# Performance work log

Measured on AMD Instinct MI355X. Metric: run time of the kernel, lower is better.

The kernel has to match this reference:

```python
import jax, jax.numpy as jnp
import numpy as np

H = 8          # n_heads
M = 16         # max_dist
U = 512        # n_units
DH = U // H    # d_head
EPS = 1e-3     # keras LayerNormalization default epsilon
NEG = -2.0**32 + 1.0


def _rel_table(pe, T):
    # pe: [2M+1, DH]; returns [T, T, DH] with rel[i, j] = pe[clip(j - i, -M, M) + M]
    i = jnp.arange(T)
    idx = jnp.clip(i[None, :] - i[:, None], -M, M) + M
    return pe[idx]


def _split_heads(x):
    # [B, T, U] -> [H*B, T, DH]  (head-major, matching tf.concat(tf.split(x, H, 2), 0))
    B, T, _ = x.shape
    return x.reshape(B, T, H, DH).transpose(2, 0, 1, 3).reshape(H * B, T, DH)


def _merge_heads(x, B):
    # [H*B, T, DH] -> [B, T, U]
    T = x.shape[1]
    return x.reshape(H, B, T, DH).transpose(1, 2, 0, 3).reshape(B, T, U)


def setup_inputs() -> dict:
    key = jax.random.key(0)
    ks = jax.random.split(key, 10)
    B, T = 8, 1024
    s = 1.0 / np.sqrt(U)
    inp = {
        'q': jax.random.normal(ks[0], (B, T, U), jnp.float32),
        'k': jax.random.normal(ks[1], (B, T, U), jnp.float32),
        'v': jax.random.normal(ks[2], (B, T, U), jnp.float32),
        'Wq': jax.random.normal(ks[3], (U, U), jnp.float32) * s,
        'bq': jnp.zeros((U,), jnp.float32),
        'Wk': jax.random.normal(ks[4], (U, U), jnp.float32) * s,
        'bk': jnp.zeros((U,), jnp.float32),
        'Wv': jax.random.normal(ks[5], (U, U), jnp.float32) * s,
        'bv': jnp.zeros((U,), jnp.float32),
        'Wo': jax.random.normal(ks[6], (U, U), jnp.float32) * s,
        'bo': jnp.zeros((U,), jnp.float32),
        'gamma': jnp.ones((U,), jnp.float32),
        'beta': jnp.zeros((U,), jnp.float32),
        'pe_k': jax.random.normal(ks[7], (2 * M + 1, DH), jnp.float32) * 0.05,
        'pe_v': jax.random.normal(ks[8], (2 * M + 1, DH), jnp.float32) * 0.05,
    }
    return inp


def reference(q, k, v, Wq, bq, Wk, bk, Wv, bv, Wo, bo, gamma, beta, pe_k, pe_v):
    B, T, _ = q.shape
    relu = jax.nn.relu
    q_emb = relu(q @ Wq + bq)
    k_emb = relu(k @ Wk + bk)
    v_emb = relu(v @ Wv + bv)
    qh = _split_heads(q_emb)   # [HB, T, DH]
    kh = _split_heads(k_emb)
    vh = _split_heads(v_emb)

    attn = jnp.einsum('btd,bsd->bts', qh, kh)
    rel_k = _rel_table(pe_k, T)                       # [T, T, DH]
    attn = attn + jnp.einsum('btd,tsd->bts', qh, rel_k)
    attn = attn / jnp.asarray(DH, attn.dtype) ** 0.5

    causal = jnp.tril(jnp.ones((T, T), jnp.bool_))
    attn = jnp.where(causal[None], attn, jnp.asarray(NEG, attn.dtype))
    w = jax.nn.softmax(attn, axis=-1)

    out = jnp.einsum('bts,bsd->btd', w, vh)
    rel_v = _rel_table(pe_v, T)
    out = out + jnp.einsum('bts,tsd->btd', w, rel_v)

    out = _merge_heads(out, B)                        # [B, T, U]
    out = relu(out @ Wo + bo)
    out = out + q

    mu = jnp.mean(out, axis=-1, keepdims=True)
    var = jnp.mean(jnp.square(out - mu), axis=-1, keepdims=True)
    return (out - mu) * jax.lax.rsqrt(var + EPS) * gamma + beta
```

## Files before the change

### kernel.cpp

```cpp
#include <hip/hip_runtime.h>
#include <hip/hip_bf16.h>

#define T_SEQ 1024
#define U_DIM 512
#define LN_EPS 1e-3f

typedef float  f32x4  __attribute__((ext_vector_type(4)));
typedef short  bf16x8 __attribute__((ext_vector_type(8)));

__device__ __forceinline__ unsigned short f2bf(float f) {
    union { float f; unsigned u; } x; x.f = f;
    unsigned r = x.u + 0x7fffu + ((x.u >> 16) & 1u);
    return (unsigned short)(r >> 16);
}
__device__ __forceinline__ float b2f(short s) {
    union { unsigned u; float f; } x; x.u = ((unsigned)(unsigned short)s) << 16;
    return x.f;
}
__device__ __forceinline__ int packbf(float a, float b) {
    return (int)((unsigned)f2bf(a) | ((unsigned)f2bf(b) << 16));
}
__device__ __forceinline__ void async_copy16(void* lds, const void* g) {
    __builtin_amdgcn_global_load_lds((const __attribute__((address_space(1))) void*)g,
                                     (__attribute__((address_space(3))) void*)lds, 16, 0, 0);
}

__global__ __launch_bounds__(256) void prep_wt(
        const float* __restrict__ Wq, const float* __restrict__ Wk,
        const float* __restrict__ Wv, const float* __restrict__ Wo,
        short* __restrict__ wt) {
    __shared__ float Ws[64][65];
    const int bid = blockIdx.x, t = threadIdx.x;
    const int z = bid >> 6, tile = bid & 63;
    const float* W = (z == 0) ? Wq : (z == 1) ? Wk : (z == 2) ? Wv : Wo;
    short* Wt = wt + (size_t)z * 262144;
    const int k0 = (tile >> 3) * 64, n0 = (tile & 7) * 64;
    {
        const int kr = t >> 2, cs = (t & 3) * 16;
        const float4* src = (const float4*)(W + (size_t)(k0 + kr) * 512 + n0 + cs);
#pragma unroll
        for (int i = 0; i < 4; ++i) {
            float4 vv = src[i];
            Ws[kr][cs + 4 * i + 0] = vv.x;
            Ws[kr][cs + 4 * i + 1] = vv.y;
            Ws[kr][cs + 4 * i + 2] = vv.z;
            Ws[kr][cs + 4 * i + 3] = vv.w;
        }
    }
    __syncthreads();
    {
        const int nr = t >> 2, ks = (t & 3) * 16;
        int4 w0, w1;
        w0.x = packbf(Ws[ks + 0][nr], Ws[ks + 1][nr]);
        w0.y = packbf(Ws[ks + 2][nr], Ws[ks + 3][nr]);
        w0.z = packbf(Ws[ks + 4][nr], Ws[ks + 5][nr]);
        w0.w = packbf(Ws[ks + 6][nr], Ws[ks + 7][nr]);
        w1.x = packbf(Ws[ks + 8][nr], Ws[ks + 9][nr]);
        w1.y = packbf(Ws[ks + 10][nr], Ws[ks + 11][nr]);
        w1.z = packbf(Ws[ks + 12][nr], Ws[ks + 13][nr]);
        w1.w = packbf(Ws[ks + 14][nr], Ws[ks + 15][nr]);
        short* dst = Wt + (size_t)(n0 + nr) * 512 + k0 + ks;
        *(int4*)dst = w0;
        *(int4*)(dst + 8) = w1;
    }
}

template <int AFP32, int OUT, int BM>
__global__ __launch_bounds__(256) void gemm_mfma(
        const void* __restrict__ A0, const void* __restrict__ A1, const void* __restrict__ A2,
        const short* __restrict__ Wt0, const short* __restrict__ Wt1, const short* __restrict__ Wt2,
        const float* __restrict__ b0p, const float* __restrict__ b1p, const float* __restrict__ b2p,
        const float* __restrict__ resid,
        void* __restrict__ O0, void* __restrict__ O1, void* __restrict__ O2) {
    constexpr int ASZ = BM * 64;
    constexpr int NW  = (BM == 128) ? 2 : 4;
    constexpr int AJ  = 8 / NW;
    constexpr int ACB = BM / 32;
    __shared__ short As[2 * ASZ];
    __shared__ short Bs[2 * 8192];

    const int z = blockIdx.z;
    const void* Av = (z == 0) ? A0 : (z == 1) ? A1 : A2;
    const short* Wz = (z == 0) ? Wt0 : (z == 1) ? Wt1 : Wt2;
    const float* bz = (z == 0) ? b0p : (z == 1) ? b1p : b2p;
    void* Ov = (z == 0) ? O0 : (z == 1) ? O1 : O2;

    const int tid = threadIdx.x;
    const int m0 = blockIdx.x * BM, n0 = blockIdx.y * 128;
    const int w = tid >> 6, lane = tid & 63;
    const int n15 = lane & 15, g = lane >> 4;
    const int mh = w / NW, nh = w % NW;
    const int lr = tid >> 4, c4 = tid & 15;

    f32x4 acc[4][AJ];
#pragma unroll
    for (int i = 0; i < 4; ++i)
#pragma unroll
        for (int j = 0; j < AJ; ++j) acc[i][j] = (f32x4){0.f, 0.f, 0.f, 0.f};

    float4 areg[8];

#define LOAD_A(CK)                                                                       \
    do {                                                                                 \
        const float* abase = (const float*)Av + (size_t)(m0 + lr) * 512 + (CK) * 64 + c4 * 4; \
        _Pragma("unroll")                                                                \
        for (int i = 0; i < 8; ++i) areg[i] = *(const float4*)(abase + (size_t)8192 * i); \
    } while (0)

#define STORE_A(BUF)                                                                     \
    do {                                                                                 \
        short* sb = As + (BUF) * ASZ + ((c4 >> 3) * (BM / 16)) * 512 + lr * 8 +          \
                    ((c4 & 7) >> 1) * 128 + (c4 & 1) * 4;                                \
        _Pragma("unroll")                                                                \
        for (int i = 0; i < 8; ++i) {                                                    \
            int2 wv;                                                                     \
            wv.x = packbf(areg[i].x, areg[i].y);                                         \
            wv.y = packbf(areg[i].z, areg[i].w);                                         \
            *(int2*)(sb + i * 512) = wv;                                                 \
        }                                                                                \
    } while (0)

#define STAGE_B(CK, BUF)                                                                 \
    do {                                                                                 \
        if (w < 2) {                                                                     \
            _Pragma("unroll")                                                            \
            for (int i = 0; i < 8; ++i) {                                                \
                const int kc = i >> 2, nt = w * 4 + (i & 3);                             \
                const short* gp = Wz + (size_t)(n0 + nt * 16 + n15) * 512 + (CK) * 64 + kc * 32 + g * 8; \
                async_copy16(Bs + (BUF) * 8192 + (kc * 8 + nt) * 512, gp);               \
            }                                                                            \
        }                                                                                \
    } while (0)

#define STAGE_A_ASYNC(CK, BUF)                                                           \
    do {                                                                                 \
        if (w >= 2) {                                                                    \
            _Pragma("unroll")                                                            \
            for (int i = 0; i < 2 * ACB; ++i) {                                          \
                const int kc = i / ACB, mt = (w - 2) * ACB + (i % ACB);                  \
                const short* gp = (const short*)Av + (size_t)(m0 + mt * 16 + n15) * 512 + (CK) * 64 + kc * 32 + g * 8; \
                async_copy16(As + (BUF) * ASZ + (kc * (BM / 16) + mt) * 512, gp);        \
            }                                                                            \
        }                                                                                \
    } while (0)

    if (AFP32) {
        LOAD_A(0);
        STORE_A(0);
        STAGE_B(0, 0);
        LOAD_A(1);
    } else {
        STAGE_B(0, 0);
        STAGE_A_ASYNC(0, 0);
    }

    for (int ck = 0; ck < 8; ++ck) {
        const int cb = ck & 1, nb = cb ^ 1;
        __syncthreads();
        if (ck < 7) {
            STAGE_B(ck + 1, nb);
            if (!AFP32) STAGE_A_ASYNC(ck + 1, nb);
        }
#pragma unroll
        for (int kc = 0; kc < 2; ++kc) {
            bf16x8 af[4], bfv[AJ];
#pragma unroll
            for (int i = 0; i < 4; ++i)
                af[i] = *(const bf16x8*)(As + cb * ASZ + (kc * (BM / 16) + mh * 4 + i) * 512 + lane * 8);
#pragma unroll
            for (int j = 0; j < AJ; ++j)
                bfv[j] = *(const bf16x8*)(Bs + cb * 8192 + (kc * 8 + nh * AJ + j) * 512 + lane * 8);
#pragma unroll
            for (int i = 0; i < 4; ++i)
#pragma unroll
                for (int j = 0; j < AJ; ++j)
                    acc[i][j] = __builtin_amdgcn_mfma_f32_16x16x32_bf16(af[i], bfv[j], acc[i][j], 0, 0, 0);
        }
        if (AFP32 && ck < 7) {
            STORE_A(nb);
            if (ck < 6) LOAD_A(ck + 2);
        }
    }
#undef LOAD_A
#undef STORE_A
#undef STAGE_B
#undef STAGE_A_ASYNC

    const int mbase = m0 + mh * 64 + g * 4;
    const int nbase = n0 + nh * (AJ * 16) + n15;
    const bool even = (n15 & 1) == 0;
    float bj[AJ];
#pragma unroll
    for (int j = 0; j < AJ; ++j) bj[j] = bz[nbase + j * 16];

#pragma unroll
    for (int i = 0; i < 4; ++i) {
        const int mrow = mbase + i * 16;
#pragma unroll
        for (int j = 0; j < AJ; ++j) {
            const int ncol = nbase + j * 16;
            f32x4 a = acc[i][j];
            float v0 = fmaxf(a[0] + bj[j], 0.f);
            float v1 = fmaxf(a[1] + bj[j], 0.f);
            float v2 = fmaxf(a[2] + bj[j], 0.f);
            float v3 = fmaxf(a[3] + bj[j], 0.f);
            if (OUT == 0) {
                unsigned t01 = (unsigned)packbf(v0, v1);
                unsigned t23 = (unsigned)packbf(v2, v3);
                unsigned x01 = (unsigned)__shfl_xor((int)t01, 1, 64);
                unsigned x23 = (unsigned)__shfl_xor((int)t23, 1, 64);
                short* Oz = (short*)Ov;
                if (even) {
                    unsigned d0 = (t01 & 0xffffu) | (x01 << 16);
                    unsigned d1 = (t01 >> 16) | (x01 & 0xffff0000u);
                    *(unsigned*)(Oz + (size_t)(mrow + 0) * 512 + ncol) = d0;
                    *(unsigned*)(Oz + (size_t)(mrow + 1) * 512 + ncol) = d1;
                } else {
                    unsigned d2 = (x23 & 0xffffu) | (t23 << 16);
                    unsigned d3 = (x23 >> 16) | (t23 & 0xffff0000u);
                    *(unsigned*)(Oz + (size_t)(mrow + 2) * 512 + ncol - 1) = d2;
                    *(unsigned*)(Oz + (size_t)(mrow + 3) * 512 + ncol - 1) = d3;
                }
            } else {
                float x0 = __shfl_xor(v0, 1, 64);
                float x1 = __shfl_xor(v1, 1, 64);
                float x2 = __shfl_xor(v2, 1, 64);
                float x3 = __shfl_xor(v3, 1, 64);
                float* Oz = (float*)Ov;
                if (even) {
                    float2 r0 = *(const float2*)(resid + (size_t)(mrow + 0) * 512 + ncol);
                    float2 r1 = *(const float2*)(resid + (size_t)(mrow + 1) * 512 + ncol);
                    *(float2*)(Oz + (size_t)(mrow + 0) * 512 + ncol) = make_float2(v0 + r0.x, x0 + r0.y);
                    *(float2*)(Oz + (size_t)(mrow + 1) * 512 + ncol) = make_float2(v1 + r1.x, x1 + r1.y);
                } else {
                    float2 r2 = *(const float2*)(resid + (size_t)(mrow + 2) * 512 + ncol - 1);
                    float2 r3 = *(const float2*)(resid + (size_t)(mrow + 3) * 512 + ncol - 1);
                    *(float2*)(Oz + (size_t)(mrow + 2) * 512 + ncol - 1) = make_float2(x2 + r2.x, v2 + r2.y);
                    *(float2*)(Oz + (size_t)(mrow + 3) * 512 + ncol - 1) = make_float2(x3 + r3.x, v3 + r3.y);
                }
            }
        }
    }
}

__global__ __launch_bounds__(256) void attn_mfma(
        const short* __restrict__ qe, const short* __restrict__ ke,
        const short* __restrict__ ve, const float* __restrict__ pe_k,
        float* __restrict__ ml, short* __restrict__ ao) {
    __shared__ short Kc[2 * 4096];
    __shared__ short Vc[2 * 4096];
    __shared__ float qpeS[4 * 16 * 17];

    const int tid = threadIdx.x;
    const int bid = blockIdx.x;
    const int rank = (bid & 3) + 4 * (bid >> 8);
    const int hb = (bid >> 2) & 63;
    const int tt = 15 - rank;
    const int h = hb >> 3, b = hb & 7;
    const int w = tid >> 6, lane = tid & 63;
    const int g = lane >> 4, n15 = lane & 15;
    const int sp = tid & 31, dbase = (tid >> 5) * 8;
    float* qpeW = qpeS + w * (16 * 17);

    const size_t rowbase = (size_t)b * T_SEQ;

    int qn = 0;
    bf16x8 Bq[2];
    float qpe0 = 0.f;
    float m_r = -3.0e38f, l_r = 0.f;
    f32x4 oacc[4];

#define SETUP(TILE)                                                                      \
    do {                                                                                 \
        qn = (TILE) * 64 + w * 16;                                                       \
        _Pragma("unroll")                                                                \
        for (int kh = 0; kh < 2; ++kh)                                                   \
            Bq[kh] = *(const bf16x8*)(qe + (rowbase + qn + n15) * U_DIM + h * 64 + kh * 32 + g * 8); \
        f32x4 qa[2];                                                                     \
        qa[0] = (f32x4){0.f, 0.f, 0.f, 0.f};                                             \
        qa[1] = (f32x4){0.f, 0.f, 0.f, 0.f};                                             \
        _Pragma("unroll")                                                                \
        for (int mt = 0; mt < 2; ++mt)                                                   \
        _Pragma("unroll")                                                                \
        for (int kh = 0; kh < 2; ++kh) {                                                 \
            const float* src = pe_k + (mt * 16 + n15) * 64 + kh * 32 + g * 8;            \
            float4 f0 = *(const float4*)src;                                             \
            float4 f1 = *(const float4*)(src + 4);                                       \
            bf16x8 fr;                                                                   \
            fr[0] = (short)f2bf(f0.x); fr[1] = (short)f2bf(f0.y);                        \
            fr[2] = (short)f2bf(f0.z); fr[3] = (short)f2bf(f0.w);                        \
            fr[4] = (short)f2bf(f1.x); fr[5] = (short)f2bf(f1.y);                        \
            fr[6] = (short)f2bf(f1.z); fr[7] = (short)f2bf(f1.w);                        \
            qa[mt] = __builtin_amdgcn_mfma_f32_16x16x32_bf16(fr, Bq[kh], qa[mt], 0, 0, 0); \
        }                                                                                \
        _Pragma("unroll")                                                                \
        for (int mt = 0; mt < 2; ++mt)                                                   \
        _Pragma("unroll")                                                                \
        for (int r = 0; r < 4; ++r) {                                                    \
            const int ri = mt * 16 + 4 * g + r;                                          \
            if (ri <= 16) qpeW[n15 * 17 + ri] = qa[mt][r];                               \
        }                                                                                \
        qpe0 = qpeW[n15 * 17];                                                           \
        m_r = -3.0e38f; l_r = 0.f;                                                       \
        _Pragma("unroll")                                                                \
        for (int dt = 0; dt < 4; ++dt) oacc[dt] = (f32x4){0.f, 0.f, 0.f, 0.f};           \
    } while (0)

#define STAGE_K(S, BUF)                                                                  \
    do {                                                                                 \
        _Pragma("unroll")                                                                \
        for (int j = 0; j < 2; ++j) {                                                    \
            const int cc = w * 2 + j, kh = cc >> 2, mt = cc & 3;                         \
            const short* gp = ke + (rowbase + (S) + mt * 16 + n15) * U_DIM + h * 64 + kh * 32 + g * 8; \
            async_copy16(Kc + (BUF) * 4096 + cc * 512, gp);                              \
        }                                                                                \
    } while (0)

#define LOAD_V(S)                                                                        \
    do {                                                                                 \
        const short* r0 = ve + (rowbase + (S) + 2 * sp) * U_DIM + h * 64 + dbase;        \
        vx = *(const bf16x8*)r0;                                                         \
        vy = *(const bf16x8*)(r0 + U_DIM);                                               \
    } while (0)

#define STORE_V(BUF)                                                                     \
    do {                                                                                 \
        const int vkh = sp >> 4, vg = (sp & 15) >> 2, vj = (sp & 3) * 2;                 \
        _Pragma("unroll")                                                                \
        for (int i = 0; i < 8; ++i) {                                                    \
            const int d = dbase + i;                                                     \
            int pv = (int)((unsigned short)vx[i]) | (((int)(unsigned short)vy[i]) << 16);\
            *(int*)(Vc + (BUF) * 4096 + (vkh * 4 + (d >> 4)) * 512 + ((d & 15) + 16 * vg) * 8 + vj) = pv; \
        }                                                                                \
    } while (0)

    SETUP(tt);
    bf16x8 vx, vy;
    STAGE_K(0, 0);
    LOAD_V(0);
    STORE_V(0);

    for (int gs = 0; gs <= tt; ++gs) {
        const int cb = gs & 1, nb = cb ^ 1;
        const int s0 = gs * 64;
        __syncthreads();
        if (gs < tt) {
            STAGE_K((gs + 1) * 64, nb);
            LOAD_V((gs + 1) * 64);
        }

        {
            int cls[4];
#pragma unroll
            for (int mt = 0; mt < 4; ++mt) {
                const int slo = s0 + mt * 16;
                cls[mt] = (slo > qn + 15) ? 0 : ((slo + 31 < qn) ? 1 : 2);
            }
            f32x4 c[4];
#pragma unroll
            for (int mt = 0; mt < 4; ++mt) c[mt] = (f32x4){0.f, 0.f, 0.f, 0.f};
#pragma unroll
            for (int mt = 0; mt < 4; ++mt) {
                if (!cls[mt]) continue;
#pragma unroll
                for (int kh = 0; kh < 2; ++kh) {
                    bf16x8 ak = *(const bf16x8*)(Kc + cb * 4096 + (kh * 4 + mt) * 512 + lane * 8);
                    c[mt] = __builtin_amdgcn_mfma_f32_16x16x32_bf16(ak, Bq[kh], c[mt], 0, 0, 0);
                }
            }

            const int qg = qn + n15;
            float sc[4][4];
            float pmax = -3.0e38f;
#pragma unroll
            for (int mt = 0; mt < 4; ++mt) {
                if (cls[mt] == 0) {
#pragma unroll
                    for (int r = 0; r < 4; ++r) sc[mt][r] = -3.0e38f;
                } else if (cls[mt] == 1) {
#pragma unroll
                    for (int r = 0; r < 4; ++r) {
                        sc[mt][r] = (c[mt][r] + qpe0) * 0.125f;
                        pmax = fmaxf(pmax, sc[mt][r]);
                    }
                } else {
#pragma unroll
                    for (int r = 0; r < 4; ++r) {
                        const int sg = s0 + mt * 16 + 4 * g + r;
                        const int dlt = sg - qg;
                        if (dlt <= 0) {
                            const int ri = (dlt < -16) ? 0 : (dlt + 16);
                            sc[mt][r] = (c[mt][r] + qpeW[n15 * 17 + ri]) * 0.125f;
                            pmax = fmaxf(pmax, sc[mt][r]);
                        } else {
                            sc[mt][r] = -3.0e38f;
                        }
                    }
                }
            }
            pmax = fmaxf(pmax, __shfl_xor(pmax, 16, 64));
            pmax = fmaxf(pmax, __shfl_xor(pmax, 32, 64));
            const float mnew = fmaxf(m_r, pmax);
            const float alpha = __expf(m_r - mnew);
            float p[4][4];
            float psum = 0.f;
#pragma unroll
            for (int mt = 0; mt < 4; ++mt)
#pragma unroll
            for (int r = 0; r < 4; ++r) {
                const float pv = (cls[mt] == 0) ? 0.f : __expf(sc[mt][r] - mnew);
                p[mt][r] = pv;
                psum += pv;
            }
            psum += __shfl_xor(psum, 16, 64);
            psum += __shfl_xor(psum, 32, 64);
            l_r = l_r * alpha + psum;
            m_r = mnew;

            int pk01[4], pk23[4];
#pragma unroll
            for (int mt = 0; mt < 4; ++mt) {
                pk01[mt] = packbf(p[mt][0], p[mt][1]);
                pk23[mt] = packbf(p[mt][2], p[mt][3]);
            }
            const int srcA = ((g & 1) * 2) * 16 + n15;
            const int srcB = srcA + 16;
            const bool selHi = (g >> 1) != 0;
            float aO[4];
#pragma unroll
            for (int r = 0; r < 4; ++r) aO[r] = __shfl(alpha, 4 * g + r, 64);
#pragma unroll
            for (int dt = 0; dt < 4; ++dt)
#pragma unroll
            for (int r = 0; r < 4; ++r) oacc[dt][r] *= aO[r];
#pragma unroll
            for (int kh = 0; kh < 2; ++kh) {
                if (cls[2 * kh] == 0 && cls[2 * kh + 1] == 0) continue;
                const int a0l = __shfl(pk01[2 * kh], srcA, 64);
                const int a0h = __shfl(pk01[2 * kh + 1], srcA, 64);
                const int a1l = __shfl(pk23[2 * kh], srcA, 64);
                const int a1h = __shfl(pk23[2 * kh + 1], srcA, 64);
                const int a2l = __shfl(pk01[2 * kh], srcB, 64);
                const int a2h = __shfl(pk01[2 * kh + 1], srcB, 64);
                const int a3l = __shfl(pk23[2 * kh], srcB, 64);
                const int a3h = __shfl(pk23[2 * kh + 1], srcB, 64);
                union { int i[4]; bf16x8 v; } au;
                au.i[0] = selHi ? a0h : a0l;
                au.i[1] = selHi ? a1h : a1l;
                au.i[2] = selHi ? a2h : a2l;
                au.i[3] = selHi ? a3h : a3l;
#pragma unroll
                for (int dt = 0; dt < 4; ++dt) {
                    bf16x8 bv = *(const bf16x8*)(Vc + cb * 4096 + (kh * 4 + dt) * 512 + lane * 8);
                    oacc[dt] = __builtin_amdgcn_mfma_f32_16x16x32_bf16(au.v, bv, oacc[dt], 0, 0, 0);
                }
            }
        }

        if (gs < tt) STORE_V(nb);
    }

    if (g == 0)
        *(float2*)(ml + ((size_t)hb * T_SEQ + qn + n15) * 2) = make_float2(m_r, l_r);
#pragma unroll
    for (int r = 0; r < 4; ++r) {
        const float lq = __shfl(l_r, 4 * g + r, 64);
        const float linv = 1.0f / lq;
        short* dst = ao + (rowbase + qn + 4 * g + r) * U_DIM + h * 64 + n15;
#pragma unroll
        for (int dt = 0; dt < 4; ++dt)
            dst[dt * 16] = (short)f2bf(oacc[dt][r] * linv);
    }
#undef SETUP
#undef STAGE_K
#undef LOAD_V
#undef STORE_V
}

__global__ __launch_bounds__(256) void band_relv(
        const short* __restrict__ qe, const short* __restrict__ ke,
        const float* __restrict__ pe_k, const float* __restrict__ pe_v,
        const float* __restrict__ ml, short* __restrict__ ao) {
    __shared__ float pek[17 * 64];
    __shared__ float pev[17 * 64];
    const int tb = blockIdx.x, hb = blockIdx.y;
    const int h = hb >> 3, b = hb & 7;
    const int tid = threadIdx.x;
    for (int i = tid; i < 17 * 64; i += 256) {
        pek[i] = b2f((short)f2bf(pe_k[i]));
        pev[i] = pe_v[i];
    }
    __syncthreads();

    const int t = tb * 64 + (tid >> 2);
    const int p = (tid & 3) * 16;
    const short* qp = qe + (size_t)(b * T_SEQ + t) * U_DIM + h * 64 + p;
    bf16x8 qa = *(const bf16x8*)qp, qb2 = *(const bf16x8*)(qp + 8);
    float qv[16];
#pragma unroll
    for (int i = 0; i < 8; ++i) { qv[i] = b2f(qa[i]); qv[8 + i] = b2f(qb2[i]); }

    float dots[17];
#pragma unroll
    for (int ri = 0; ri < 17; ++ri) {
        const int s = t - 16 + ri;
        float acc = 0.f;
        if (s >= 0) {
            const short* kp = ke + (size_t)(b * T_SEQ + s) * U_DIM + h * 64 + p;
            bf16x8 ka = *(const bf16x8*)kp, kb2 = *(const bf16x8*)(kp + 8);
#pragma unroll
            for (int d = 0; d < 8; ++d) {
                acc += qv[d] * b2f(ka[d]);
                acc += qv[8 + d] * b2f(kb2[d]);
            }
#pragma unroll
            for (int d = 0; d < 16; ++d) acc += qv[d] * pek[ri * 64 + p + d];
        }
        dots[ri] = acc;
    }
#pragma unroll
    for (int ri = 0; ri < 17; ++ri) {
        dots[ri] += __shfl_xor(dots[ri], 1, 64);
        dots[ri] += __shfl_xor(dots[ri], 2, 64);
    }

    const float2 mlv = *(const float2*)(ml + ((size_t)hb * T_SEQ + t) * 2);
    const float m = mlv.x, linv = 1.0f / mlv.y;
    float wv[17];
    float wsum = 0.f;
#pragma unroll
    for (int ri = 0; ri < 17; ++ri) {
        const int s = t - 16 + ri;
        const float wr = (s >= 0) ? __expf(dots[ri] * 0.125f - m) * linv : 0.f;
        wv[ri] = wr;
        wsum += wr;
    }
    wv[0] += 1.0f - wsum;

    float relv[16];
#pragma unroll
    for (int d = 0; d < 16; ++d) relv[d] = 0.f;
#pragma unroll
    for (int ri = 0; ri < 17; ++ri)
#pragma unroll
        for (int d = 0; d < 16; ++d) relv[d] += wv[ri] * pev[ri * 64 + p + d];

    short* op = ao + (size_t)(b * T_SEQ + t) * U_DIM + h * 64 + p;
    bf16x8 a0 = *(const bf16x8*)op, a1 = *(const bf16x8*)(op + 8);
    int4 o0, o1;
    o0.x = packbf(b2f(a0[0]) + relv[0],  b2f(a0[1]) + relv[1]);
    o0.y = packbf(b2f(a0[2]) + relv[2],  b2f(a0[3]) + relv[3]);
    o0.z = packbf(b2f(a0[4]) + relv[4],  b2f(a0[5]) + relv[5]);
    o0.w = packbf(b2f(a0[6]) + relv[6],  b2f(a0[7]) + relv[7]);
    o1.x = packbf(b2f(a1[0]) + relv[8],  b2f(a1[1]) + relv[9]);
    o1.y = packbf(b2f(a1[2]) + relv[10], b2f(a1[3]) + relv[11]);
    o1.z = packbf(b2f(a1[4]) + relv[12], b2f(a1[5]) + relv[13]);
    o1.w = packbf(b2f(a1[6]) + relv[14], b2f(a1[7]) + relv[15]);
    *(int4*)op = o0;
    *(int4*)(op + 8) = o1;
}

__global__ __launch_bounds__(256) void ln_kernel(float* __restrict__ io,
                                                 const float* __restrict__ gamma,
                                                 const float* __restrict__ beta) {
    const int row = blockIdx.x * 4 + (threadIdx.x >> 6);
    const int lane = threadIdx.x & 63;
    float* rp = io + (size_t)row * 512 + lane * 8;
    float4 a = *(const float4*)rp;
    float4 c = *(const float4*)(rp + 4);
    float v[8] = {a.x, a.y, a.z, a.w, c.x, c.y, c.z, c.w};

    float s = v[0] + v[1] + v[2] + v[3] + v[4] + v[5] + v[6] + v[7];
#pragma unroll
    for (int off = 1; off < 64; off <<= 1) s += __shfl_xor(s, off, 64);
    const float mu = s * (1.0f / 512.0f);

    float sq = 0.f;
#pragma unroll
    for (int i = 0; i < 8; ++i) { v[i] -= mu; sq += v[i] * v[i]; }
#pragma unroll
    for (int off = 1; off < 64; off <<= 1) sq += __shfl_xor(sq, off, 64);
    const float rs = rsqrtf(sq * (1.0f / 512.0f) + LN_EPS);

    const float4 g0 = *(const float4*)(gamma + lane * 8);
    const float4 g1 = *(const float4*)(gamma + lane * 8 + 4);
    const float4 b0 = *(const float4*)(beta + lane * 8);
    const float4 b1 = *(const float4*)(beta + lane * 8 + 4);
    float4 o0, o1;
    o0.x = v[0] * rs * g0.x + b0.x;
    o0.y = v[1] * rs * g0.y + b0.y;
    o0.z = v[2] * rs * g0.z + b0.z;
    o0.w = v[3] * rs * g0.w + b0.w;
    o1.x = v[4] * rs * g1.x + b1.x;
    o1.y = v[5] * rs * g1.y + b1.y;
    o1.z = v[6] * rs * g1.z + b1.z;
    o1.w = v[7] * rs * g1.w + b1.w;
    *(float4*)rp = o0;
    *(float4*)(rp + 4) = o1;
}

extern "C" void kernel_launch(void* const* d_in, const int* in_sizes, int n_in,
                              void* d_out, int out_size, void* d_ws, size_t ws_size,
                              hipStream_t stream) {
    const float* q     = (const float*)d_in[0];
    const float* k     = (const float*)d_in[1];
    const float* v     = (const float*)d_in[2];
    const float* Wq    = (const float*)d_in[3];
    const float* bq    = (const float*)d_in[4];
    const float* Wk    = (const float*)d_in[5];
    const float* bk    = (const float*)d_in[6];
    const float* Wv    = (const float*)d_in[7];
    const float* bv    = (const float*)d_in[8];
    const float* Wo    = (const float*)d_in[9];
    const float* bo    = (const float*)d_in[10];
    const float* gamma = (const float*)d_in[11];
    const float* beta  = (const float*)d_in[12];
    const float* pe_k  = (const float*)d_in[13];
    const float* pe_v  = (const float*)d_in[14];
    float* out = (float*)d_out;

    char* base = (char*)d_ws;
    short* qe = (short*)(base);
    short* ke = (short*)(base + (((size_t)8) << 20));
    short* ve = (short*)(base + (((size_t)16) << 20));
    short* ao = (short*)(base + (((size_t)24) << 20));
    short* wt = (short*)(base + (((size_t)32) << 20));
    float* ml = (float*)(base + (((size_t)34) << 20));
    short* wtq = wt, *wtk = wt + 262144, *wtv = wt + 2 * 262144, *wto = wt + 3 * 262144;

    prep_wt<<<dim3(256), 256, 0, stream>>>(Wq, Wk, Wv, Wo, wt);
    gemm_mfma<1, 0, 128><<<dim3(64, 4, 3), 256, 0, stream>>>(
        q, k, v, wtq, wtk, wtv, bq, bk, bv, nullptr, qe, ke, ve);
    attn_mfma<<<dim3(1024), 256, 0, stream>>>(qe, ke, ve, pe_k, ml, ao);
    band_relv<<<dim3(16, 64), 256, 0, stream>>>(qe, ke, pe_k, pe_v, ml, ao);
    gemm_mfma<0, 1, 64><<<dim3(128, 4, 1), 256, 0, stream>>>(
        ao, ao, ao, wto, wto, wto, bo, bo, bo, q, out, out, out);
    ln_kernel<<<dim3(2048), 256, 0, stream>>>(out, gamma, beta);
}
```

Before: 240.2 us.

## Pre-convert QKV inputs to bf16 and use async LDS staging with narrower N tiles

Adds a separate kernel that converts q, k, v from fp32 to bf16 in a workspace. The QKV projection GEMM can then drop its register-staged fp32 load and convert path and use the same async global-to-LDS copies as the output GEMM. The GEMM is generalized over BN, and the QKV launch uses BN=64 with twice as many blocks in N. The cost is an extra kernel launch plus an extra fp32 read and bf16 write of 3x16 MB of activations.

```diff
diff --git a/kernel.cpp b/kernel.cpp
--- a/kernel.cpp
+++ b/kernel.cpp
@@ -23,6 +23,25 @@
 __device__ __forceinline__ void async_copy16(void* lds, const void* g) {
     __builtin_amdgcn_global_load_lds((const __attribute__((address_space(1))) void*)g,
                                      (__attribute__((address_space(3))) void*)lds, 16, 0, 0);
+}
+
+__global__ __launch_bounds__(256) void conv_bf16(
+        const float* __restrict__ q, const float* __restrict__ k, const float* __restrict__ v,
+        short* __restrict__ qb, short* __restrict__ kb, short* __restrict__ vb) {
+    const size_t off = ((size_t)blockIdx.x * 256 + threadIdx.x) * 8;
+#pragma unroll
+    for (int z = 0; z < 3; ++z) {
+        const float* src = (z == 0) ? q : (z == 1) ? k : v;
+        short* dst = (z == 0) ? qb : (z == 1) ? kb : vb;
+        float4 a = *(const float4*)(src + off);
+        float4 b = *(const float4*)(src + off + 4);
+        int4 o;
+        o.x = packbf(a.x, a.y);
+        o.y = packbf(a.z, a.w);
+        o.z = packbf(b.x, b.y);
+        o.w = packbf(b.z, b.w);
+        *(int4*)(dst + off) = o;
+    }
 }
 
 __global__ __launch_bounds__(256) void prep_wt(
@@ -65,7 +84,7 @@
     }
 }
 
-template <int AFP32, int OUT, int BM>
+template <int OUT, int BM, int BN>
 __global__ __launch_bounds__(256) void gemm_mfma(
         const void* __restrict__ A0, const void* __restrict__ A1, const void* __restrict__ A2,
         const short* __restrict__ Wt0, const short* __restrict__ Wt1, const short* __restrict__ Wt2,
@@ -73,11 +92,15 @@
         const float* __restrict__ resid,
         void* __restrict__ O0, void* __restrict__ O1, void* __restrict__ O2) {
     constexpr int ASZ = BM * 64;
-    constexpr int NW  = (BM == 128) ? 2 : 4;
-    constexpr int AJ  = 8 / NW;
+    constexpr int BSZ = BN * 64;
+    constexpr int MW  = BM / 64;
+    constexpr int NW  = 4 / MW;
+    constexpr int AJ  = BN / (16 * NW);
+    constexpr int BNC = BN / 16;
+    constexpr int NTW = BNC / 2;
     constexpr int ACB = BM / 32;
     __shared__ short As[2 * ASZ];
-    __shared__ short Bs[2 * 8192];
+    __shared__ short Bs[2 * BSZ];
 
     const int z = blockIdx.z;
     const void* Av = (z == 0) ? A0 : (z == 1) ? A1 : A2;
@@ -86,53 +109,30 @@
     void* Ov = (z == 0) ? O0 : (z == 1) ? O1 : O2;
 
     const int tid = threadIdx.x;
-    const int m0 = blockIdx.x * BM, n0 = blockIdx.y * 128;
+    const int m0 = blockIdx.x * BM, n0 = blockIdx.y * BN;
     const int w = tid >> 6, lane = tid & 63;
     const int n15 = lane & 15, g = lane >> 4;
     const int mh = w / NW, nh = w % NW;
-    const int lr = tid >> 4, c4 = tid & 15;
 
     f32x4 acc[4][AJ];
 #pragma unroll
     for (int i = 0; i < 4; ++i)
 #pragma unroll
         for (int j = 0; j < AJ; ++j) acc[i][j] = (f32x4){0.f, 0.f, 0.f, 0.f};
-
-    float4 areg[8];
-
-#define LOAD_A(CK)                                                                       \
-    do {                                                                                 \
-        const float* abase = (const float*)Av + (size_t)(m0 + lr) * 512 + (CK) * 64 + c4 * 4; \
-        _Pragma("unroll")                                                                \
-        for (int i = 0; i < 8; ++i) areg[i] = *(const float4*)(abase + (size_t)8192 * i); \
-    } while (0)
-
-#define STORE_A(BUF)                                                                     \
-    do {                                                                                 \
-        short* sb = As + (BUF) * ASZ + ((c4 >> 3) * (BM / 16)) * 512 + lr * 8 +          \
-                    ((c4 & 7) >> 1) * 128 + (c4 & 1) * 4;                                \
-        _Pragma("unroll")                                                                \
-        for (int i = 0; i < 8; ++i) {                                                    \
-            int2 wv;                                                                     \
-            wv.x = packbf(areg[i].x, areg[i].y);                                         \
-            wv.y = packbf(areg[i].z, areg[i].w);                                         \
-            *(int2*)(sb + i * 512) = wv;                                                 \
-        }                                                                                \
-    } while (0)
 
 #define STAGE_B(CK, BUF)                                                                 \
     do {                                                                                 \
         if (w < 2) {                                                                     \
             _Pragma("unroll")                                                            \
-            for (int i = 0; i < 8; ++i) {                                                \
-                const int kc = i >> 2, nt = w * 4 + (i & 3);                             \
+            for (int i = 0; i < 2 * NTW; ++i) {                                          \
+                const int kc = i / NTW, nt = w * NTW + (i % NTW);                        \
                 const short* gp = Wz + (size_t)(n0 + nt * 16 + n15) * 512 + (CK) * 64 + kc * 32 + g * 8; \
-                async_copy16(Bs + (BUF) * 8192 + (kc * 8 + nt) * 512, gp);               \
+                async_copy16(Bs + (BUF) * BSZ + (kc * BNC + nt) * 512, gp);              \
             }                                                                            \
         }                                                                                \
     } while (0)
 
-#define STAGE_A_ASYNC(CK, BUF)                                                           \
+#define STAGE_A(CK, BUF)                                                                 \
     do {                                                                                 \
         if (w >= 2) {                                                                    \
             _Pragma("unroll")                                                            \
@@ -144,22 +144,15 @@
         }                                                                                \
     } while (0)
 
-    if (AFP32) {
-        LOAD_A(0);
-        STORE_A(0);
-        STAGE_B(0, 0);
-        LOAD_A(1);
-    } else {
-        STAGE_B(0, 0);
-        STAGE_A_ASYNC(0, 0);
-    }
+    STAGE_B(0, 0);
+    STAGE_A(0, 0);
 
     for (int ck = 0; ck < 8; ++ck) {
         const int cb = ck & 1, nb = cb ^ 1;
         __syncthreads();
         if (ck < 7) {
             STAGE_B(ck + 1, nb);
-            if (!AFP32) STAGE_A_ASYNC(ck + 1, nb);
+            STAGE_A(ck + 1, nb);
         }
 #pragma unroll
         for (int kc = 0; kc < 2; ++kc) {
@@ -169,22 +162,16 @@
                 af[i] = *(const bf16x8*)(As + cb * ASZ + (kc * (BM / 16) + mh * 4 + i) * 512 + lane * 8);
 #pragma unroll
             for (int j = 0; j < AJ; ++j)
-                bfv[j] = *(const bf16x8*)(Bs + cb * 8192 + (kc * 8 + nh * AJ + j) * 512 + lane * 8);
+                bfv[j] = *(const bf16x8*)(Bs + cb * BSZ + (kc * BNC + nh * AJ + j) * 512 + lane * 8);
 #pragma unroll
             for (int i = 0; i < 4; ++i)
 #pragma unroll
                 for (int j = 0; j < AJ; ++j)
                     acc[i][j] = __builtin_amdgcn_mfma_f32_16x16x32_bf16(af[i], bfv[j], acc[i][j], 0, 0, 0);
         }
-        if (AFP32 && ck < 7) {
-            STORE_A(nb);
-            if (ck < 6) LOAD_A(ck + 2);
-        }
-    }
-#undef LOAD_A
-#undef STORE_A
+    }
 #undef STAGE_B
-#undef STAGE_A_ASYNC
+#undef STAGE_A
 
     const int mbase = m0 + mh * 64 + g * 4;
     const int nbase = n0 + nh * (AJ * 16) + n15;
@@ -626,14 +613,18 @@
     short* ao = (short*)(base + (((size_t)24) << 20));
     short* wt = (short*)(base + (((size_t)32) << 20));
     float* ml = (float*)(base + (((size_t)34) << 20));
+    short* qb = (short*)(base + (((size_t)36) << 20));
+    short* kb = (short*)(base + (((size_t)44) << 20));
+    short* vb = (short*)(base + (((size_t)52) << 20));
     short* wtq = wt, *wtk = wt + 262144, *wtv = wt + 2 * 262144, *wto = wt + 3 * 262144;
 
     prep_wt<<<dim3(256), 256, 0, stream>>>(Wq, Wk, Wv, Wo, wt);
-    gemm_mfma<1, 0, 128><<<dim3(64, 4, 3), 256, 0, stream>>>(
-        q, k, v, wtq, wtk, wtv, bq, bk, bv, nullptr, qe, ke, ve);
+    conv_bf16<<<dim3(2048), 256, 0, stream>>>(q, k, v, qb, kb, vb);
+    gemm_mfma<0, 128, 64><<<dim3(64, 8, 3), 256, 0, stream>>>(
+        qb, kb, vb, wtq, wtk, wtv, bq, bk, bv, nullptr, qe, ke, ve);
     attn_mfma<<<dim3(1024), 256, 0, stream>>>(qe, ke, ve, pe_k, ml, ao);
     band_relv<<<dim3(16, 64), 256, 0, stream>>>(qe, ke, pe_k, pe_v, ml, ao);
-    gemm_mfma<0, 1, 64><<<dim3(128, 4, 1), 256, 0, stream>>>(
+    gemm_mfma<1, 64, 128><<<dim3(128, 4, 1), 256, 0, stream>>>(
         ao, ao, ao, wto, wto, wto, bo, bo, bo, q, out, out, out);
     ln_kernel<<<dim3(2048), 256, 0, stream>>>(out, gamma, beta);
 }
```

After: 253.6 us. +5.6%, slower.
